# Kernel tuning notes

Hardware: AMD Instinct MI355X
Metric: run time of the kernel (lower is better)

Reference implementation:

```python
import jax, jax.numpy as jnp
import numpy as np

DT = 0.001  # forward-arg default in the original module
EPS = 1e-10


def setup_inputs() -> dict:
    key = jax.random.key(0)
    k1, k2 = jax.random.split(key)
    x = jax.random.normal(k1, (5000, 512, 16), dtype=jnp.float32)  # [nt, traces, channels]
    y = jax.random.normal(k2, (5000, 512, 16), dtype=jnp.float32)
    return {"x": x, "y": y}


def reference(x, y):
    # Per-(t,c) L2 norms over time axis (dim 0): shape [T, C]
    xnorm = jnp.linalg.norm(x, ord=2, axis=0) + EPS
    ynorm = jnp.linalg.norm(y, ord=2, axis=0) + EPS
    # Per-(t,c) dot products over time: shape [T, C]
    dots = jnp.einsum('ntc,ntc->tc', x, y)
    # cc = -dot(xn * dt, yn) = -dt * dot(x, y) / (||x|| * ||y||)
    cc = -DT * dots / (xnorm * ynorm)
    # Original skips slices where max|x| == 0 (contributes 0.0)
    mask = jnp.max(jnp.abs(x), axis=0) > 0
    return jnp.sum(jnp.where(mask, cc, jnp.zeros_like(cc)))
```

## Files before the change

kernel.cpp:

```cpp
#include <hip/hip_runtime.h>
#include <hip/hip_bf16.h>
#include <math.h>


#define NT       5000
#define NROW_F   8192
#define NCOL     8192
#define NCOL4    2048

typedef __attribute__((address_space(3))) void lds_void;
typedef const __attribute__((address_space(1))) void gm_void;

__global__ __launch_bounds__(256) void ncc_partial(const float* __restrict__ xg,
                                                   const float* __restrict__ yg,
                                                   float4* __restrict__ ws,
                                                   int clen, int nchunk, int T) {
    __shared__ float4 BA[4][4][2][64];
    __shared__ float4 BB[4][4][2][64];

    const int tid  = threadIdx.x;
    const int w    = tid >> 6;
    const int lane = tid & 63;
    const int bx   = blockIdx.x;
    const int ch   = blockIdx.y;
    const int n0   = ch * clen;
    int n1 = n0 + clen; if (n1 > NT) n1 = NT;

    const int colf = bx * 1024 + tid * 4;

    float4 sxx = make_float4(0.f, 0.f, 0.f, 0.f);
    float4 syy = make_float4(0.f, 0.f, 0.f, 0.f);
    float4 sxy = make_float4(0.f, 0.f, 0.f, 0.f);
    float4 mx  = make_float4(0.f, 0.f, 0.f, 0.f);

#define ACC4(a, b)                                                      \
    sxx.x = fmaf(a.x, a.x, sxx.x); sxx.y = fmaf(a.y, a.y, sxx.y);       \
    sxx.z = fmaf(a.z, a.z, sxx.z); sxx.w = fmaf(a.w, a.w, sxx.w);       \
    syy.x = fmaf(b.x, b.x, syy.x); syy.y = fmaf(b.y, b.y, syy.y);       \
    syy.z = fmaf(b.z, b.z, syy.z); syy.w = fmaf(b.w, b.w, syy.w);       \
    sxy.x = fmaf(a.x, b.x, sxy.x); sxy.y = fmaf(a.y, b.y, sxy.y);       \
    sxy.z = fmaf(a.z, b.z, sxy.z); sxy.w = fmaf(a.w, b.w, sxy.w);       \
    mx.x = fmaxf(mx.x, fabsf(a.x)); mx.y = fmaxf(mx.y, fabsf(a.y));     \
    mx.z = fmaxf(mx.z, fabsf(a.z)); mx.w = fmaxf(mx.w, fabsf(a.w))

#define ISSUE(BUF, t)                                                         \
    {                                                                         \
        _Pragma("unroll")                                                     \
        for (int r = 0; r < 4; ++r) {                                         \
            int n = n0 + (t) * 4 + r;                                         \
            if (n > NT - 1) n = NT - 1;                                       \
            const float* px = xg + (size_t)n * NROW_F + colf;                 \
            const float* py = yg + (size_t)n * NROW_F + colf;                 \
            __builtin_amdgcn_global_load_lds((gm_void*)px,                    \
                (lds_void*)&BUF[w][r][0][0], 16, 0, 0);                       \
            __builtin_amdgcn_global_load_lds((gm_void*)py,                    \
                (lds_void*)&BUF[w][r][1][0], 16, 0, 0);                       \
        }                                                                     \
    }

#define COMPUTE(BUF, t)                                                       \
    {                                                                         \
        _Pragma("unroll")                                                     \
        for (int r = 0; r < 4; ++r) {                                         \
            float4 a = BUF[w][r][0][lane];                                    \
            float4 b = BUF[w][r][1][lane];                                    \
            int n = n0 + (t) * 4 + r;                                         \
            if (n < n1) { ACC4(a, b); }                                       \
        }                                                                     \
    }

#define WAITV(N)                                                              \
    asm volatile("s_waitcnt vmcnt(" #N ")" ::: "memory");                     \
    __builtin_amdgcn_sched_barrier(0)

#define WAITL()                                                               \
    asm volatile("s_waitcnt lgkmcnt(0)" ::: "memory");                        \
    __builtin_amdgcn_sched_barrier(0)

    ISSUE(BA, 0);
    ISSUE(BB, 1);
    for (int t = 0; t + 4 <= T; t += 2) {
        WAITV(8);
        COMPUTE(BA, t);
        WAITL();
        ISSUE(BA, t + 2);
        WAITV(8);
        COMPUTE(BB, t + 1);
        WAITL();
        ISSUE(BB, t + 3);
    }
    WAITV(8);
    COMPUTE(BA, T - 2);
    WAITV(0);
    COMPUTE(BB, T - 1);

#undef ACC4
#undef ISSUE
#undef COMPUTE
#undef WAITV
#undef WAITL

    float4* SXX = ws;
    float4* SYY = ws + (size_t)nchunk * NCOL4;
    float4* SXY = ws + (size_t)2 * nchunk * NCOL4;
    float4* MX  = ws + (size_t)3 * nchunk * NCOL4;
    const size_t idx = (size_t)ch * NCOL4 + bx * 256 + tid;
    SXX[idx] = sxx;
    SYY[idx] = syy;
    SXY[idx] = sxy;
    MX[idx]  = mx;
}

__global__ __launch_bounds__(256) void ncc_combine(const float4* __restrict__ ws4,
                                                   float* __restrict__ partials,
                                                   int nchunk) {
    const int lane  = threadIdx.x & 63;
    const int strip = threadIdx.x >> 6;
    const int c4    = blockIdx.x * 64 + lane;

    const float4* SXX = ws4;
    const float4* SYY = ws4 + (size_t)nchunk * NCOL4;
    const float4* SXY = ws4 + (size_t)2 * nchunk * NCOL4;
    const float4* MX  = ws4 + (size_t)3 * nchunk * NCOL4;

    const int spc = (nchunk + 3) / 4;
    int ch0 = strip * spc;
    int ch1 = ch0 + spc;
    if (ch1 > nchunk) ch1 = nchunk;

    float4 sxx = make_float4(0.f, 0.f, 0.f, 0.f);
    float4 syy = make_float4(0.f, 0.f, 0.f, 0.f);
    float4 sxy = make_float4(0.f, 0.f, 0.f, 0.f);
    float4 mx  = make_float4(0.f, 0.f, 0.f, 0.f);
    for (int ch = ch0; ch < ch1; ++ch) {
        const size_t idx = (size_t)ch * NCOL4 + c4;
        float4 a = SXX[idx], b = SYY[idx], d = SXY[idx], m = MX[idx];
        sxx.x += a.x; sxx.y += a.y; sxx.z += a.z; sxx.w += a.w;
        syy.x += b.x; syy.y += b.y; syy.z += b.z; syy.w += b.w;
        sxy.x += d.x; sxy.y += d.y; sxy.z += d.z; sxy.w += d.w;
        mx.x = fmaxf(mx.x, m.x); mx.y = fmaxf(mx.y, m.y);
        mx.z = fmaxf(mx.z, m.z); mx.w = fmaxf(mx.w, m.w);
    }

    __shared__ float4 LXX[4][64], LYY[4][64], LXY[4][64], LMX[4][64];
    LXX[strip][lane] = sxx;
    LYY[strip][lane] = syy;
    LXY[strip][lane] = sxy;
    LMX[strip][lane] = mx;
    __syncthreads();

    if (strip == 0) {
        for (int s = 1; s < 4; ++s) {
            float4 a = LXX[s][lane], b = LYY[s][lane], d = LXY[s][lane], m = LMX[s][lane];
            sxx.x += a.x; sxx.y += a.y; sxx.z += a.z; sxx.w += a.w;
            syy.x += b.x; syy.y += b.y; syy.z += b.z; syy.w += b.w;
            sxy.x += d.x; sxy.y += d.y; sxy.z += d.z; sxy.w += d.w;
            mx.x = fmaxf(mx.x, m.x); mx.y = fmaxf(mx.y, m.y);
            mx.z = fmaxf(mx.z, m.z); mx.w = fmaxf(mx.w, m.w);
        }
        float cc = 0.f;
        if (mx.x > 0.f) cc += -0.001f * sxy.x / ((sqrtf(sxx.x) + 1e-10f) * (sqrtf(syy.x) + 1e-10f));
        if (mx.y > 0.f) cc += -0.001f * sxy.y / ((sqrtf(sxx.y) + 1e-10f) * (sqrtf(syy.y) + 1e-10f));
        if (mx.z > 0.f) cc += -0.001f * sxy.z / ((sqrtf(sxx.z) + 1e-10f) * (sqrtf(syy.z) + 1e-10f));
        if (mx.w > 0.f) cc += -0.001f * sxy.w / ((sqrtf(sxx.w) + 1e-10f) * (sqrtf(syy.w) + 1e-10f));

        for (int off = 32; off > 0; off >>= 1)
            cc += __shfl_down(cc, off);
        if (lane == 0)
            partials[blockIdx.x] = cc;
    }
}

__global__ __launch_bounds__(64) void ncc_final(const float* __restrict__ partials,
                                                float* __restrict__ out) {
    float v = (threadIdx.x < 32) ? partials[threadIdx.x] : 0.f;
    for (int off = 32; off > 0; off >>= 1)
        v += __shfl_down(v, off);
    if (threadIdx.x == 0) out[0] = v;
}

extern "C" void kernel_launch(void* const* d_in, const int* in_sizes, int n_in,
                              void* d_out, int out_size, void* d_ws, size_t ws_size,
                              hipStream_t stream) {
    const float* x = (const float*)d_in[0];
    const float* y = (const float*)d_in[1];
    float* out = (float*)d_out;
    float* ws  = (float*)d_ws;

    const size_t per_chunk_bytes = 4ull * NCOL * sizeof(float);
    size_t avail = (ws_size > 256) ? (ws_size - 256) : 0;
    int nchunk = (int)(avail / per_chunk_bytes);
    if (nchunk > 64) nchunk = 64;
    if (nchunk < 1)  nchunk = 1;
    const int clen = (NT + nchunk - 1) / nchunk;

    int T = (clen + 3) / 4;
    if (T & 1) T++;
    if (T < 2) T = 2;

    float* partials = ws + 4ull * (size_t)nchunk * NCOL;

    dim3 g1(8, nchunk);
    ncc_partial<<<g1, 256, 0, stream>>>(x, y, (float4*)ws, clen, nchunk, T);
    ncc_combine<<<32, 256, 0, stream>>>((const float4*)ws, partials, nchunk);
    ncc_final<<<1, 64, 0, stream>>>(partials, out);
}
```

Before: 67.38 us.

## Double chunk count, halve rows per stage, widen combine to 1024 threads

Raises the cap on time chunks from 64 to 128, giving up to 1024 partial blocks, and halves the rows loaded per pipeline stage (2 instead of 4) with matching vmcnt waits. The combine kernel now uses 64 blocks of 1024 threads, with 32 strips and an LDS tree reduction, and the final kernel sums 64 partials. The aim is more parallelism on the bandwidth-bound pass over 330MB. In exchange each wave has fewer loads in flight, and the workspace of partial sums is twice as large.

Measured after the change: 71.63 us. 1.06x slower.

```diff
diff --git a/kernel.cpp b/kernel.cpp
--- a/kernel.cpp
+++ b/kernel.cpp
@@ -15,8 +15,8 @@
                                                    const float* __restrict__ yg,
                                                    float4* __restrict__ ws,
                                                    int clen, int nchunk, int T) {
-    __shared__ float4 BA[4][4][2][64];
-    __shared__ float4 BB[4][4][2][64];
+    __shared__ float4 BA[4][2][2][64];
+    __shared__ float4 BB[4][2][2][64];
 
     const int tid  = threadIdx.x;
     const int w    = tid >> 6;
@@ -46,8 +46,8 @@
 #define ISSUE(BUF, t)                                                         \
     {                                                                         \
         _Pragma("unroll")                                                     \
-        for (int r = 0; r < 4; ++r) {                                         \
-            int n = n0 + (t) * 4 + r;                                         \
+        for (int r = 0; r < 2; ++r) {                                         \
+            int n = n0 + (t) * 2 + r;                                         \
             if (n > NT - 1) n = NT - 1;                                       \
             const float* px = xg + (size_t)n * NROW_F + colf;                 \
             const float* py = yg + (size_t)n * NROW_F + colf;                 \
@@ -61,10 +61,10 @@
 #define COMPUTE(BUF, t)                                                       \
     {                                                                         \
         _Pragma("unroll")                                                     \
-        for (int r = 0; r < 4; ++r) {                                         \
+        for (int r = 0; r < 2; ++r) {                                         \
             float4 a = BUF[w][r][0][lane];                                    \
             float4 b = BUF[w][r][1][lane];                                    \
-            int n = n0 + (t) * 4 + r;                                         \
+            int n = n0 + (t) * 2 + r;                                         \
             if (n < n1) { ACC4(a, b); }                                       \
         }                                                                     \
     }
@@ -80,16 +80,16 @@
     ISSUE(BA, 0);
     ISSUE(BB, 1);
     for (int t = 0; t + 4 <= T; t += 2) {
-        WAITV(8);
+        WAITV(4);
         COMPUTE(BA, t);
         WAITL();
         ISSUE(BA, t + 2);
-        WAITV(8);
+        WAITV(4);
         COMPUTE(BB, t + 1);
         WAITL();
         ISSUE(BB, t + 3);
     }
-    WAITV(8);
+    WAITV(4);
     COMPUTE(BA, T - 2);
     WAITV(0);
     COMPUTE(BB, T - 1);
@@ -111,19 +111,19 @@
     MX[idx]  = mx;
 }
 
-__global__ __launch_bounds__(256) void ncc_combine(const float4* __restrict__ ws4,
-                                                   float* __restrict__ partials,
-                                                   int nchunk) {
-    const int lane  = threadIdx.x & 63;
-    const int strip = threadIdx.x >> 6;
-    const int c4    = blockIdx.x * 64 + lane;
+__global__ __launch_bounds__(1024) void ncc_combine(const float4* __restrict__ ws4,
+                                                    float* __restrict__ partials,
+                                                    int nchunk) {
+    const int c4l   = threadIdx.x & 31;
+    const int strip = threadIdx.x >> 5;
+    const int c4    = blockIdx.x * 32 + c4l;
 
     const float4* SXX = ws4;
     const float4* SYY = ws4 + (size_t)nchunk * NCOL4;
     const float4* SXY = ws4 + (size_t)2 * nchunk * NCOL4;
     const float4* MX  = ws4 + (size_t)3 * nchunk * NCOL4;
 
-    const int spc = (nchunk + 3) / 4;
+    const int spc = (nchunk + 31) >> 5;
     int ch0 = strip * spc;
     int ch1 = ch0 + spc;
     if (ch1 > nchunk) ch1 = nchunk;
@@ -142,38 +142,52 @@
         mx.z = fmaxf(mx.z, m.z); mx.w = fmaxf(mx.w, m.w);
     }
 
-    __shared__ float4 LXX[4][64], LYY[4][64], LXY[4][64], LMX[4][64];
-    LXX[strip][lane] = sxx;
-    LYY[strip][lane] = syy;
-    LXY[strip][lane] = sxy;
-    LMX[strip][lane] = mx;
+    __shared__ float4 L[32][4][32];
+    L[strip][0][c4l] = sxx;
+    L[strip][1][c4l] = syy;
+    L[strip][2][c4l] = sxy;
+    L[strip][3][c4l] = mx;
     __syncthreads();
 
+    for (int s = 16; s >= 1; s >>= 1) {
+        if (strip < s) {
+            float4 a0 = L[strip][0][c4l], a1 = L[strip + s][0][c4l];
+            float4 b0 = L[strip][1][c4l], b1 = L[strip + s][1][c4l];
+            float4 d0 = L[strip][2][c4l], d1 = L[strip + s][2][c4l];
+            float4 m0 = L[strip][3][c4l], m1 = L[strip + s][3][c4l];
+            a0.x += a1.x; a0.y += a1.y; a0.z += a1.z; a0.w += a1.w;
+            b0.x += b1.x; b0.y += b1.y; b0.z += b1.z; b0.w += b1.w;
+            d0.x += d1.x; d0.y += d1.y; d0.z += d1.z; d0.w += d1.w;
+            m0.x = fmaxf(m0.x, m1.x); m0.y = fmaxf(m0.y, m1.y);
+            m0.z = fmaxf(m0.z, m1.z); m0.w = fmaxf(m0.w, m1.w);
+            L[strip][0][c4l] = a0;
+            L[strip][1][c4l] = b0;
+            L[strip][2][c4l] = d0;
+            L[strip][3][c4l] = m0;
+        }
+        __syncthreads();
+    }
+
     if (strip == 0) {
-        for (int s = 1; s < 4; ++s) {
-            float4 a = LXX[s][lane], b = LYY[s][lane], d = LXY[s][lane], m = LMX[s][lane];
-            sxx.x += a.x; sxx.y += a.y; sxx.z += a.z; sxx.w += a.w;
-            syy.x += b.x; syy.y += b.y; syy.z += b.z; syy.w += b.w;
-            sxy.x += d.x; sxy.y += d.y; sxy.z += d.z; sxy.w += d.w;
-            mx.x = fmaxf(mx.x, m.x); mx.y = fmaxf(mx.y, m.y);
-            mx.z = fmaxf(mx.z, m.z); mx.w = fmaxf(mx.w, m.w);
-        }
+        sxx = L[0][0][c4l];
+        syy = L[0][1][c4l];
+        sxy = L[0][2][c4l];
+        mx  = L[0][3][c4l];
         float cc = 0.f;
         if (mx.x > 0.f) cc += -0.001f * sxy.x / ((sqrtf(sxx.x) + 1e-10f) * (sqrtf(syy.x) + 1e-10f));
         if (mx.y > 0.f) cc += -0.001f * sxy.y / ((sqrtf(sxx.y) + 1e-10f) * (sqrtf(syy.y) + 1e-10f));
         if (mx.z > 0.f) cc += -0.001f * sxy.z / ((sqrtf(sxx.z) + 1e-10f) * (sqrtf(syy.z) + 1e-10f));
         if (mx.w > 0.f) cc += -0.001f * sxy.w / ((sqrtf(sxx.w) + 1e-10f) * (sqrtf(syy.w) + 1e-10f));
-
-        for (int off = 32; off > 0; off >>= 1)
+        for (int off = 16; off > 0; off >>= 1)
             cc += __shfl_down(cc, off);
-        if (lane == 0)
+        if (c4l == 0)
             partials[blockIdx.x] = cc;
     }
 }
 
 __global__ __launch_bounds__(64) void ncc_final(const float* __restrict__ partials,
                                                 float* __restrict__ out) {
-    float v = (threadIdx.x < 32) ? partials[threadIdx.x] : 0.f;
+    float v = partials[threadIdx.x];
     for (int off = 32; off > 0; off >>= 1)
         v += __shfl_down(v, off);
     if (threadIdx.x == 0) out[0] = v;
@@ -188,13 +202,13 @@
     float* ws  = (float*)d_ws;
 
     const size_t per_chunk_bytes = 4ull * NCOL * sizeof(float);
-    size_t avail = (ws_size > 256) ? (ws_size - 256) : 0;
+    size_t avail = (ws_size > 512) ? (ws_size - 512) : 0;
     int nchunk = (int)(avail / per_chunk_bytes);
-    if (nchunk > 64) nchunk = 64;
-    if (nchunk < 1)  nchunk = 1;
+    if (nchunk > 128) nchunk = 128;
+    if (nchunk < 1)   nchunk = 1;
     const int clen = (NT + nchunk - 1) / nchunk;
 
-    int T = (clen + 3) / 4;
+    int T = (clen + 1) / 2;
     if (T & 1) T++;
     if (T < 2) T = 2;
 
@@ -202,6 +216,6 @@
 
     dim3 g1(8, nchunk);
     ncc_partial<<<g1, 256, 0, stream>>>(x, y, (float4*)ws, clen, nchunk, T);
-    ncc_combine<<<32, 256, 0, stream>>>((const float4*)ws, partials, nchunk);
+    ncc_combine<<<64, 1024, 0, stream>>>((const float4*)ws, partials, nchunk);
     ncc_final<<<1, 64, 0, stream>>>(partials, out);
 }
```
